# Optimization experiments

Measured on AMD Instinct MI355X. Metric: run time of the kernel, lower is better.

Reference implementation:

```python
import jax, jax.numpy as jnp
import numpy as np

WINDOW_SIZE = 11
SIGMA = 1.5
C1 = 0.01 ** 2
C2 = 0.03 ** 2


def _gaussian_window(channel, window_size=WINDOW_SIZE, sigma=SIGMA):
    # Faithful to the torch code: the 1D gaussian is NOT normalized.
    x = jnp.arange(window_size, dtype=jnp.float32)
    g = jnp.exp(-((x - window_size // 2) ** 2) / (2.0 * sigma ** 2))
    w2d = jnp.outer(g, g)  # [ws, ws]
    return jnp.broadcast_to(w2d[None, None], (channel, 1, window_size, window_size))


def _dwconv(x, window, window_size, channel):
    # depthwise conv2d with SAME-ish padding = window_size // 2
    pad = window_size // 2
    return jax.lax.conv_general_dilated(
        x, window,
        window_strides=(1, 1),
        padding=[(pad, pad), (pad, pad)],
        dimension_numbers=("NCHW", "OIHW", "NCHW"),
        feature_group_count=channel,
    )


def setup_inputs() -> dict:
    key = jax.random.key(0)
    k1, k2 = jax.random.split(key)
    B, C, H, W = 16, 3, 512, 512
    img1 = jax.random.uniform(k1, (B, C, H, W), dtype=jnp.float32)
    img2 = jax.random.uniform(k2, (B, C, H, W), dtype=jnp.float32)
    return {"img1": img1, "img2": img2}


def reference(img1, img2):
    channel = img1.shape[1]
    window = _gaussian_window(channel).astype(img1.dtype)

    mu1 = _dwconv(img1, window, WINDOW_SIZE, channel)
    mu2 = _dwconv(img2, window, WINDOW_SIZE, channel)
    mu1_sq = mu1 * mu1
    mu2_sq = mu2 * mu2
    mu1_mu2 = mu1 * mu2

    sigma1_sq = _dwconv(img1 * img1, window, WINDOW_SIZE, channel) - mu1_sq
    sigma2_sq = _dwconv(img2 * img2, window, WINDOW_SIZE, channel) - mu2_sq
    sigma12 = _dwconv(img1 * img2, window, WINDOW_SIZE, channel) - mu1_mu2

    ssim_map = ((2.0 * mu1_mu2 + C1) * (2.0 * sigma12 + C2)) / (
        (mu1_sq + mu2_sq + C1) * (sigma1_sq + sigma2_sq + C2)
    )
    # size_average=True -> scalar mean
    return 1.0 - jnp.mean(ssim_map)
```

## Files before the change

kernel.cpp:

```cpp
#include <hip/hip_runtime.h>


#define IMG   512
#define NIMG  48
#define TW    32
#define TH    32
#define PH    42
#define PWS   44
#define TILES 16
#define NBLOCKS (NIMG * TILES * TILES)

#define G0 0.0038659204f
#define G1 0.0285655010f
#define G2 0.1353352832f
#define G3 0.4111123050f
#define G4 0.8007374029f
#define G5 1.0f

__global__ __launch_bounds__(256, 5) void ssim_tile_kernel(
    const float* __restrict__ img1, const float* __restrict__ img2,
    float* __restrict__ partials)
{
    __shared__ float s1[PH][PWS];
    __shared__ float s2[PH][PWS];
    __shared__ float sh[3][TW][PWS];
    __shared__ float s_part[4];

    const float gw[11] = {G0,G1,G2,G3,G4,G5,G4,G3,G2,G1,G0};

    const int tid = threadIdx.x;
    const int tx0 = blockIdx.x * TW - 5;
    const int ty0 = blockIdx.y * TH - 5;
    const float* __restrict__ p1 = img1 + (size_t)blockIdx.z * (IMG * IMG);
    const float* __restrict__ p2 = img2 + (size_t)blockIdx.z * (IMG * IMG);

    {
        int r = tid / 42;
        int c = tid - r * 42;
#pragma unroll
        for (int it = 0; it < 7; ++it) {
            if (it < 6 || r < PH) {
                int gr = ty0 + r, gc = tx0 + c;
                bool ok = ((unsigned)gr < IMG) && ((unsigned)gc < IMG);
                int gi = gr * IMG + gc;
                s1[r][c] = ok ? p1[gi] : 0.0f;
                s2[r][c] = ok ? p2[gi] : 0.0f;
            }
            c += 4; r += 6;
            if (c >= 42) { c -= 42; r += 1; }
        }
    }

    const bool hact = tid < 168;
    const int  hr  = hact ? (tid % 42) : 0;
    const int  hc0 = hact ? ((tid / 42) * 8) : 0;

    const int col = tid & 31;
    const int r0  = (tid >> 5) * 4;

    __syncthreads();

    if (hact) {
        float v1[20];
#pragma unroll
        for (int q = 0; q < 5; ++q)
            *(float4*)&v1[4 * q] = *(const float4*)&s1[hr][hc0 + 4 * q];
        float m1[8], q11[8];
#pragma unroll
        for (int j = 0; j < 8; ++j) { m1[j] = 0.f; q11[j] = 0.f; }
#pragma unroll
        for (int k = 0; k < 11; ++k) {
            float w = gw[k];
#pragma unroll
            for (int j = 0; j < 8; ++j) {
                float a = v1[j + k];
                float t = w * a;
                m1[j] += t;
                q11[j] = fmaf(t, a, q11[j]);
            }
        }
#pragma unroll
        for (int j = 0; j < 8; ++j) {
            sh[0][hc0 + j][hr] = m1[j];
            sh[1][hc0 + j][hr] = q11[j];
        }
    }
    __syncthreads();

    float a_m1[4], a_q11[4];
    {
        float h[16];
#pragma unroll
        for (int ch = 0; ch < 2; ++ch) {
            const float* b = &sh[ch][col][0];
#pragma unroll
            for (int q = 0; q < 4; ++q)
                *(float4*)&h[4 * q] = *(const float4*)&b[r0 + 4 * q];
            float* acc = ch ? a_q11 : a_m1;
#pragma unroll
            for (int i = 0; i < 4; ++i) {
                float s = 0.f;
#pragma unroll
                for (int k = 0; k < 11; ++k) s = fmaf(gw[k], h[i + k], s);
                acc[i] = s;
            }
        }
    }
    __syncthreads();

    if (hact) {
        float v1[20], v2[20];
#pragma unroll
        for (int q = 0; q < 5; ++q) {
            *(float4*)&v1[4 * q] = *(const float4*)&s1[hr][hc0 + 4 * q];
            *(float4*)&v2[4 * q] = *(const float4*)&s2[hr][hc0 + 4 * q];
        }
        float m2[8], q22[8], q12[8];
#pragma unroll
        for (int j = 0; j < 8; ++j) { m2[j] = 0.f; q22[j] = 0.f; q12[j] = 0.f; }
#pragma unroll
        for (int k = 0; k < 11; ++k) {
            float w = gw[k];
#pragma unroll
            for (int j = 0; j < 8; ++j) {
                float b = v2[j + k];
                float t = w * b;
                m2[j] += t;
                q22[j] = fmaf(t, b, q22[j]);
                q12[j] = fmaf(t, v1[j + k], q12[j]);
            }
        }
#pragma unroll
        for (int j = 0; j < 8; ++j) {
            sh[0][hc0 + j][hr] = m2[j];
            sh[1][hc0 + j][hr] = q22[j];
            sh[2][hc0 + j][hr] = q12[j];
        }
    }
    __syncthreads();

    float a_m2[4], a_q22[4], a_q12[4];
    {
        float h[16];
#pragma unroll
        for (int ch = 0; ch < 3; ++ch) {
            const float* b = &sh[ch][col][0];
#pragma unroll
            for (int q = 0; q < 4; ++q)
                *(float4*)&h[4 * q] = *(const float4*)&b[r0 + 4 * q];
            float* acc = (ch == 0) ? a_m2 : (ch == 1) ? a_q22 : a_q12;
#pragma unroll
            for (int i = 0; i < 4; ++i) {
                float s = 0.f;
#pragma unroll
                for (int k = 0; k < 11; ++k) s = fmaf(gw[k], h[i + k], s);
                acc[i] = s;
            }
        }
    }

    const float C1 = 1.0e-4f, C2 = 9.0e-4f;
    float local = 0.f;
#pragma unroll
    for (int i = 0; i < 4; ++i) {
        float mu1 = a_m1[i], mu2 = a_m2[i];
        float mu1s = mu1 * mu1, mu2s = mu2 * mu2, m12 = mu1 * mu2;
        float sg1 = a_q11[i] - mu1s, sg2 = a_q22[i] - mu2s, sg12 = a_q12[i] - m12;
        float num = (2.f * m12 + C1) * (2.f * sg12 + C2);
        float den = (mu1s + mu2s + C1) * (sg1 + sg2 + C2);
        local = fmaf(num, __builtin_amdgcn_rcpf(den), local);
    }

#pragma unroll
    for (int off = 32; off > 0; off >>= 1)
        local += __shfl_down(local, off, 64);
    if ((tid & 63) == 0) s_part[tid >> 6] = local;
    __syncthreads();
    if (tid == 0) {
        int bidx = (blockIdx.z * gridDim.y + blockIdx.y) * gridDim.x + blockIdx.x;
        partials[bidx] = s_part[0] + s_part[1] + s_part[2] + s_part[3];
    }
}

__global__ __launch_bounds__(256) void ssim_final_kernel(
    const float* __restrict__ partials, float* __restrict__ out)
{
    __shared__ double sp[4];
    double acc = 0.0;
    for (int i = threadIdx.x; i < NBLOCKS; i += 256)
        acc += (double)partials[i];
#pragma unroll
    for (int off = 32; off > 0; off >>= 1)
        acc += __shfl_down(acc, off, 64);
    if ((threadIdx.x & 63) == 0) sp[threadIdx.x >> 6] = acc;
    __syncthreads();
    if (threadIdx.x == 0) {
        double total = sp[0] + sp[1] + sp[2] + sp[3];
        out[0] = (float)(1.0 - total / (double)((size_t)NIMG * IMG * IMG));
    }
}

extern "C" void kernel_launch(void* const* d_in, const int* in_sizes, int n_in,
                              void* d_out, int out_size, void* d_ws, size_t ws_size,
                              hipStream_t stream) {
    const float* img1 = (const float*)d_in[0];
    const float* img2 = (const float*)d_in[1];
    float* out = (float*)d_out;
    float* partials = (float*)d_ws;

    dim3 grid(TILES, TILES, NIMG);
    ssim_tile_kernel<<<grid, dim3(256), 0, stream>>>(img1, img2, partials);
    ssim_final_kernel<<<1, dim3(256), 0, stream>>>(partials, out);
}
```

Before: 189.3 us.

## Filter sum and difference images to cut SSIM convolution channels from five to four

Result: faster. 165.3 us (-12.7%).

```diff
diff --git a/kernel.cpp b/kernel.cpp
--- a/kernel.cpp
+++ b/kernel.cpp
@@ -17,13 +17,13 @@
 #define G4 0.8007374029f
 #define G5 1.0f
 
-__global__ __launch_bounds__(256, 5) void ssim_tile_kernel(
+__global__ __launch_bounds__(256, 6) void ssim_tile_kernel(
     const float* __restrict__ img1, const float* __restrict__ img2,
     float* __restrict__ partials)
 {
-    __shared__ float s1[PH][PWS];
-    __shared__ float s2[PH][PWS];
-    __shared__ float sh[3][TW][PWS];
+    __shared__ float ssm[PH][PWS];
+    __shared__ float sdf[PH][PWS];
+    __shared__ float sh[2][TW][PWS];
     __shared__ float s_part[4];
 
     const float gw[11] = {G0,G1,G2,G3,G4,G5,G4,G3,G2,G1,G0};
@@ -35,19 +35,37 @@
     const float* __restrict__ p2 = img2 + (size_t)blockIdx.z * (IMG * IMG);
 
     {
+        const bool interior = (blockIdx.x >= 1) && (blockIdx.x <= TILES - 2) &&
+                              (blockIdx.y >= 1) && (blockIdx.y <= TILES - 2);
         int r = tid / 42;
         int c = tid - r * 42;
-#pragma unroll
-        for (int it = 0; it < 7; ++it) {
-            if (it < 6 || r < PH) {
-                int gr = ty0 + r, gc = tx0 + c;
-                bool ok = ((unsigned)gr < IMG) && ((unsigned)gc < IMG);
-                int gi = gr * IMG + gc;
-                s1[r][c] = ok ? p1[gi] : 0.0f;
-                s2[r][c] = ok ? p2[gi] : 0.0f;
-            }
-            c += 4; r += 6;
-            if (c >= 42) { c -= 42; r += 1; }
+        if (interior) {
+#pragma unroll
+            for (int it = 0; it < 7; ++it) {
+                if (it < 6 || r < PH) {
+                    int gi = (ty0 + r) * IMG + (tx0 + c);
+                    float a = p1[gi], b = p2[gi];
+                    ssm[r][c] = a + b;
+                    sdf[r][c] = a - b;
+                }
+                c += 4; r += 6;
+                if (c >= 42) { c -= 42; r += 1; }
+            }
+        } else {
+#pragma unroll
+            for (int it = 0; it < 7; ++it) {
+                if (it < 6 || r < PH) {
+                    int gr = ty0 + r, gc = tx0 + c;
+                    bool ok = ((unsigned)gr < IMG) && ((unsigned)gc < IMG);
+                    int gi = gr * IMG + gc;
+                    float a = ok ? p1[gi] : 0.0f;
+                    float b = ok ? p2[gi] : 0.0f;
+                    ssm[r][c] = a + b;
+                    sdf[r][c] = a - b;
+                }
+                c += 4; r += 6;
+                if (c >= 42) { c -= 42; r += 1; }
+            }
         }
     }
 
@@ -58,104 +76,114 @@
     const int col = tid & 31;
     const int r0  = (tid >> 5) * 4;
 
+    float a_ms[4], a_xss[4], a_md[4], a_xdd[4];
+
     __syncthreads();
 
     if (hact) {
-        float v1[20];
+        float v[20];
 #pragma unroll
         for (int q = 0; q < 5; ++q)
-            *(float4*)&v1[4 * q] = *(const float4*)&s1[hr][hc0 + 4 * q];
-        float m1[8], q11[8];
-#pragma unroll
-        for (int j = 0; j < 8; ++j) { m1[j] = 0.f; q11[j] = 0.f; }
+            *(float4*)&v[4 * q] = *(const float4*)&ssm[hr][hc0 + 4 * q];
+        float m[8], x[8];
+#pragma unroll
+        for (int j = 0; j < 8; ++j) { m[j] = 0.f; x[j] = 0.f; }
 #pragma unroll
         for (int k = 0; k < 11; ++k) {
             float w = gw[k];
 #pragma unroll
             for (int j = 0; j < 8; ++j) {
-                float a = v1[j + k];
+                float a = v[j + k];
                 float t = w * a;
-                m1[j] += t;
-                q11[j] = fmaf(t, a, q11[j]);
-            }
-        }
+                m[j] += t;
+                x[j] = fmaf(t, a, x[j]);
+            }
+        }
+        float* sb = &sh[0][hc0][hr];
 #pragma unroll
         for (int j = 0; j < 8; ++j) {
-            sh[0][hc0 + j][hr] = m1[j];
-            sh[1][hc0 + j][hr] = q11[j];
-        }
-    }
-    __syncthreads();
-
-    float a_m1[4], a_q11[4];
+            sb[j * PWS] = m[j];
+            sb[TW * PWS + j * PWS] = x[j];
+        }
+    }
+    __syncthreads();
+
     {
+        const float* vb = &sh[0][col][r0];
         float h[16];
 #pragma unroll
-        for (int ch = 0; ch < 2; ++ch) {
-            const float* b = &sh[ch][col][0];
-#pragma unroll
-            for (int q = 0; q < 4; ++q)
-                *(float4*)&h[4 * q] = *(const float4*)&b[r0 + 4 * q];
-            float* acc = ch ? a_q11 : a_m1;
-#pragma unroll
-            for (int i = 0; i < 4; ++i) {
-                float s = 0.f;
-#pragma unroll
-                for (int k = 0; k < 11; ++k) s = fmaf(gw[k], h[i + k], s);
-                acc[i] = s;
-            }
+        for (int q = 0; q < 4; ++q)
+            *(float4*)&h[4 * q] = *(const float4*)&vb[4 * q];
+#pragma unroll
+        for (int i = 0; i < 4; ++i) {
+            float s = 0.f;
+#pragma unroll
+            for (int k = 0; k < 11; ++k) s = fmaf(gw[k], h[i + k], s);
+            a_ms[i] = s;
+        }
+#pragma unroll
+        for (int q = 0; q < 4; ++q)
+            *(float4*)&h[4 * q] = *(const float4*)&vb[TW * PWS + 4 * q];
+#pragma unroll
+        for (int i = 0; i < 4; ++i) {
+            float s = 0.f;
+#pragma unroll
+            for (int k = 0; k < 11; ++k) s = fmaf(gw[k], h[i + k], s);
+            a_xss[i] = s;
         }
     }
     __syncthreads();
 
     if (hact) {
-        float v1[20], v2[20];
-#pragma unroll
-        for (int q = 0; q < 5; ++q) {
-            *(float4*)&v1[4 * q] = *(const float4*)&s1[hr][hc0 + 4 * q];
-            *(float4*)&v2[4 * q] = *(const float4*)&s2[hr][hc0 + 4 * q];
-        }
-        float m2[8], q22[8], q12[8];
-#pragma unroll
-        for (int j = 0; j < 8; ++j) { m2[j] = 0.f; q22[j] = 0.f; q12[j] = 0.f; }
+        float v[20];
+#pragma unroll
+        for (int q = 0; q < 5; ++q)
+            *(float4*)&v[4 * q] = *(const float4*)&sdf[hr][hc0 + 4 * q];
+        float m[8], x[8];
+#pragma unroll
+        for (int j = 0; j < 8; ++j) { m[j] = 0.f; x[j] = 0.f; }
 #pragma unroll
         for (int k = 0; k < 11; ++k) {
             float w = gw[k];
 #pragma unroll
             for (int j = 0; j < 8; ++j) {
-                float b = v2[j + k];
-                float t = w * b;
-                m2[j] += t;
-                q22[j] = fmaf(t, b, q22[j]);
-                q12[j] = fmaf(t, v1[j + k], q12[j]);
-            }
-        }
+                float a = v[j + k];
+                float t = w * a;
+                m[j] += t;
+                x[j] = fmaf(t, a, x[j]);
+            }
+        }
+        float* sb = &sh[0][hc0][hr];
 #pragma unroll
         for (int j = 0; j < 8; ++j) {
-            sh[0][hc0 + j][hr] = m2[j];
-            sh[1][hc0 + j][hr] = q22[j];
-            sh[2][hc0 + j][hr] = q12[j];
-        }
-    }
-    __syncthreads();
-
-    float a_m2[4], a_q22[4], a_q12[4];
+            sb[j * PWS] = m[j];
+            sb[TW * PWS + j * PWS] = x[j];
+        }
+    }
+    __syncthreads();
+
     {
+        const float* vb = &sh[0][col][r0];
         float h[16];
 #pragma unroll
-        for (int ch = 0; ch < 3; ++ch) {
-            const float* b = &sh[ch][col][0];
-#pragma unroll
-            for (int q = 0; q < 4; ++q)
-                *(float4*)&h[4 * q] = *(const float4*)&b[r0 + 4 * q];
-            float* acc = (ch == 0) ? a_m2 : (ch == 1) ? a_q22 : a_q12;
-#pragma unroll
-            for (int i = 0; i < 4; ++i) {
-                float s = 0.f;
-#pragma unroll
-                for (int k = 0; k < 11; ++k) s = fmaf(gw[k], h[i + k], s);
-                acc[i] = s;
-            }
+        for (int q = 0; q < 4; ++q)
+            *(float4*)&h[4 * q] = *(const float4*)&vb[4 * q];
+#pragma unroll
+        for (int i = 0; i < 4; ++i) {
+            float s = 0.f;
+#pragma unroll
+            for (int k = 0; k < 11; ++k) s = fmaf(gw[k], h[i + k], s);
+            a_md[i] = s;
+        }
+#pragma unroll
+        for (int q = 0; q < 4; ++q)
+            *(float4*)&h[4 * q] = *(const float4*)&vb[TW * PWS + 4 * q];
+#pragma unroll
+        for (int i = 0; i < 4; ++i) {
+            float s = 0.f;
+#pragma unroll
+            for (int k = 0; k < 11; ++k) s = fmaf(gw[k], h[i + k], s);
+            a_xdd[i] = s;
         }
     }
 
@@ -163,11 +191,17 @@
     float local = 0.f;
 #pragma unroll
     for (int i = 0; i < 4; ++i) {
-        float mu1 = a_m1[i], mu2 = a_m2[i];
-        float mu1s = mu1 * mu1, mu2s = mu2 * mu2, m12 = mu1 * mu2;
-        float sg1 = a_q11[i] - mu1s, sg2 = a_q22[i] - mu2s, sg12 = a_q12[i] - m12;
+        float ms = a_ms[i], md = a_md[i];
+        float xss = a_xss[i], xdd = a_xdd[i];
+        float ms2 = ms * ms, md2 = md * md;
+        float sum2 = 0.5f * (ms2 + md2);
+        float m12  = 0.25f * (ms2 - md2);
+        float xsum = 0.5f * (xss + xdd);
+        float x12  = 0.25f * (xss - xdd);
+        float sg12 = x12 - m12;
+        float sgsum = xsum - sum2;
         float num = (2.f * m12 + C1) * (2.f * sg12 + C2);
-        float den = (mu1s + mu2s + C1) * (sg1 + sg2 + C2);
+        float den = (sum2 + C1) * (sgsum + C2);
         local = fmaf(num, __builtin_amdgcn_rcpf(den), local);
     }
 
```

## Reformulate SSIM via sum/difference images with packed float2 convolutions

Applied to the files above, without the earlier changes.

Result: faster. 169.3 us (-10.6%).

```diff
diff --git a/kernel.cpp b/kernel.cpp
--- a/kernel.cpp
+++ b/kernel.cpp
@@ -1,12 +1,15 @@
 #include <hip/hip_runtime.h>
 
+
+typedef float v2f __attribute__((ext_vector_type(2)));
 
 #define IMG   512
 #define NIMG  48
 #define TW    32
 #define TH    32
 #define PH    42
-#define PWS   44
+#define SSTR  46
+#define HSTR  46
 #define TILES 16
 #define NBLOCKS (NIMG * TILES * TILES)
 
@@ -17,13 +20,12 @@
 #define G4 0.8007374029f
 #define G5 1.0f
 
-__global__ __launch_bounds__(256, 5) void ssim_tile_kernel(
+__global__ __launch_bounds__(256, 4) void ssim_tile_kernel(
     const float* __restrict__ img1, const float* __restrict__ img2,
     float* __restrict__ partials)
 {
-    __shared__ float s1[PH][PWS];
-    __shared__ float s2[PH][PWS];
-    __shared__ float sh[3][TW][PWS];
+    __shared__ v2f ssd[PH][SSTR];
+    __shared__ v2f sh2[2][TW][HSTR];
     __shared__ float s_part[4];
 
     const float gw[11] = {G0,G1,G2,G3,G4,G5,G4,G3,G2,G1,G0};
@@ -35,19 +37,35 @@
     const float* __restrict__ p2 = img2 + (size_t)blockIdx.z * (IMG * IMG);
 
     {
+        const bool interior = (blockIdx.x >= 1) && (blockIdx.x <= TILES - 2) &&
+                              (blockIdx.y >= 1) && (blockIdx.y <= TILES - 2);
         int r = tid / 42;
         int c = tid - r * 42;
-#pragma unroll
-        for (int it = 0; it < 7; ++it) {
-            if (it < 6 || r < PH) {
-                int gr = ty0 + r, gc = tx0 + c;
-                bool ok = ((unsigned)gr < IMG) && ((unsigned)gc < IMG);
-                int gi = gr * IMG + gc;
-                s1[r][c] = ok ? p1[gi] : 0.0f;
-                s2[r][c] = ok ? p2[gi] : 0.0f;
-            }
-            c += 4; r += 6;
-            if (c >= 42) { c -= 42; r += 1; }
+        if (interior) {
+#pragma unroll
+            for (int it = 0; it < 7; ++it) {
+                if (it < 6 || r < PH) {
+                    int gi = (ty0 + r) * IMG + (tx0 + c);
+                    float a = p1[gi], b = p2[gi];
+                    ssd[r][c] = (v2f){a + b, a - b};
+                }
+                c += 4; r += 6;
+                if (c >= 42) { c -= 42; r += 1; }
+            }
+        } else {
+#pragma unroll
+            for (int it = 0; it < 7; ++it) {
+                if (it < 6 || r < PH) {
+                    int gr = ty0 + r, gc = tx0 + c;
+                    bool ok = ((unsigned)gr < IMG) && ((unsigned)gc < IMG);
+                    int gi = gr * IMG + gc;
+                    float a = ok ? p1[gi] : 0.0f;
+                    float b = ok ? p2[gi] : 0.0f;
+                    ssd[r][c] = (v2f){a + b, a - b};
+                }
+                c += 4; r += 6;
+                if (c >= 42) { c -= 42; r += 1; }
+            }
         }
     }
 
@@ -61,101 +79,73 @@
     __syncthreads();
 
     if (hact) {
-        float v1[20];
-#pragma unroll
-        for (int q = 0; q < 5; ++q)
-            *(float4*)&v1[4 * q] = *(const float4*)&s1[hr][hc0 + 4 * q];
-        float m1[8], q11[8];
-#pragma unroll
-        for (int j = 0; j < 8; ++j) { m1[j] = 0.f; q11[j] = 0.f; }
+        v2f v[20];
+        {
+            const float4* src = (const float4*)&ssd[hr][hc0];
+#pragma unroll
+            for (int q = 0; q < 10; ++q) ((float4*)v)[q] = src[q];
+        }
+        v2f m[8];
+#pragma unroll
+        for (int j = 0; j < 8; ++j) m[j] = (v2f){0.f, 0.f};
 #pragma unroll
         for (int k = 0; k < 11; ++k) {
-            float w = gw[k];
-#pragma unroll
-            for (int j = 0; j < 8; ++j) {
-                float a = v1[j + k];
-                float t = w * a;
-                m1[j] += t;
-                q11[j] = fmaf(t, a, q11[j]);
-            }
-        }
-#pragma unroll
-        for (int j = 0; j < 8; ++j) {
-            sh[0][hc0 + j][hr] = m1[j];
-            sh[1][hc0 + j][hr] = q11[j];
-        }
-    }
-    __syncthreads();
-
-    float a_m1[4], a_q11[4];
+            const v2f wv = {gw[k], gw[k]};
+#pragma unroll
+            for (int j = 0; j < 8; ++j)
+                m[j] = __builtin_elementwise_fma(v[j + k], wv, m[j]);
+        }
+#pragma unroll
+        for (int j = 0; j < 8; ++j) sh2[0][hc0 + j][hr] = m[j];
+#pragma unroll
+        for (int e = 0; e < 18; ++e) v[e] *= v[e];
+        v2f x[8];
+#pragma unroll
+        for (int j = 0; j < 8; ++j) x[j] = (v2f){0.f, 0.f};
+#pragma unroll
+        for (int k = 0; k < 11; ++k) {
+            const v2f wv = {gw[k], gw[k]};
+#pragma unroll
+            for (int j = 0; j < 8; ++j)
+                x[j] = __builtin_elementwise_fma(v[j + k], wv, x[j]);
+        }
+#pragma unroll
+        for (int j = 0; j < 8; ++j) sh2[1][hc0 + j][hr] = x[j];
+    }
+    __syncthreads();
+
+    v2f am[4], ax[4];
     {
-        float h[16];
-#pragma unroll
-        for (int ch = 0; ch < 2; ++ch) {
-            const float* b = &sh[ch][col][0];
-#pragma unroll
-            for (int q = 0; q < 4; ++q)
-                *(float4*)&h[4 * q] = *(const float4*)&b[r0 + 4 * q];
-            float* acc = ch ? a_q11 : a_m1;
-#pragma unroll
-            for (int i = 0; i < 4; ++i) {
-                float s = 0.f;
-#pragma unroll
-                for (int k = 0; k < 11; ++k) s = fmaf(gw[k], h[i + k], s);
-                acc[i] = s;
-            }
-        }
-    }
-    __syncthreads();
-
-    if (hact) {
-        float v1[20], v2[20];
-#pragma unroll
-        for (int q = 0; q < 5; ++q) {
-            *(float4*)&v1[4 * q] = *(const float4*)&s1[hr][hc0 + 4 * q];
-            *(float4*)&v2[4 * q] = *(const float4*)&s2[hr][hc0 + 4 * q];
-        }
-        float m2[8], q22[8], q12[8];
-#pragma unroll
-        for (int j = 0; j < 8; ++j) { m2[j] = 0.f; q22[j] = 0.f; q12[j] = 0.f; }
-#pragma unroll
-        for (int k = 0; k < 11; ++k) {
-            float w = gw[k];
-#pragma unroll
-            for (int j = 0; j < 8; ++j) {
-                float b = v2[j + k];
-                float t = w * b;
-                m2[j] += t;
-                q22[j] = fmaf(t, b, q22[j]);
-                q12[j] = fmaf(t, v1[j + k], q12[j]);
-            }
-        }
-#pragma unroll
-        for (int j = 0; j < 8; ++j) {
-            sh[0][hc0 + j][hr] = m2[j];
-            sh[1][hc0 + j][hr] = q22[j];
-            sh[2][hc0 + j][hr] = q12[j];
-        }
-    }
-    __syncthreads();
-
-    float a_m2[4], a_q22[4], a_q12[4];
-    {
-        float h[16];
-#pragma unroll
-        for (int ch = 0; ch < 3; ++ch) {
-            const float* b = &sh[ch][col][0];
-#pragma unroll
-            for (int q = 0; q < 4; ++q)
-                *(float4*)&h[4 * q] = *(const float4*)&b[r0 + 4 * q];
-            float* acc = (ch == 0) ? a_m2 : (ch == 1) ? a_q22 : a_q12;
-#pragma unroll
-            for (int i = 0; i < 4; ++i) {
-                float s = 0.f;
-#pragma unroll
-                for (int k = 0; k < 11; ++k) s = fmaf(gw[k], h[i + k], s);
-                acc[i] = s;
-            }
+        v2f hb[16];
+        {
+            const float4* s0 = (const float4*)&sh2[0][col][r0];
+#pragma unroll
+            for (int q = 0; q < 8; ++q) ((float4*)hb)[q] = s0[q];
+        }
+#pragma unroll
+        for (int i = 0; i < 4; ++i) {
+            v2f s = {0.f, 0.f};
+#pragma unroll
+            for (int k = 0; k < 11; ++k) {
+                const v2f wv = {gw[k], gw[k]};
+                s = __builtin_elementwise_fma(wv, hb[i + k], s);
+            }
+            am[i] = s;
+        }
+        {
+            const float4* s1 = (const float4*)&sh2[1][col][r0];
+#pragma unroll
+            for (int q = 0; q < 8; ++q) ((float4*)hb)[q] = s1[q];
+        }
+#pragma unroll
+        for (int i = 0; i < 4; ++i) {
+            v2f s = {0.f, 0.f};
+#pragma unroll
+            for (int k = 0; k < 11; ++k) {
+                const v2f wv = {gw[k], gw[k]};
+                s = __builtin_elementwise_fma(wv, hb[i + k], s);
+            }
+            ax[i] = s;
         }
     }
 
@@ -163,11 +153,17 @@
     float local = 0.f;
 #pragma unroll
     for (int i = 0; i < 4; ++i) {
-        float mu1 = a_m1[i], mu2 = a_m2[i];
-        float mu1s = mu1 * mu1, mu2s = mu2 * mu2, m12 = mu1 * mu2;
-        float sg1 = a_q11[i] - mu1s, sg2 = a_q22[i] - mu2s, sg12 = a_q12[i] - m12;
+        v2f mu = am[i];
+        v2f mu2 = mu * mu;
+        float sum2 = 0.5f  * (mu2[0] + mu2[1]);
+        float m12  = 0.25f * (mu2[0] - mu2[1]);
+        v2f xx = ax[i];
+        float xsum = 0.5f  * (xx[0] + xx[1]);
+        float x12  = 0.25f * (xx[0] - xx[1]);
+        float sg12  = x12 - m12;
+        float sgsum = xsum - sum2;
         float num = (2.f * m12 + C1) * (2.f * sg12 + C2);
-        float den = (mu1s + mu2s + C1) * (sg1 + sg2 + C2);
+        float den = (sum2 + C1) * (sgsum + C2);
         local = fmaf(num, __builtin_amdgcn_rcpf(den), local);
     }
 
```
